# Optimization experiments

Hardware: AMD Instinct MI355X
Metric: run time of the kernel (lower is better)

The kernel has to match this reference:

```python
import jax, jax.numpy as jnp
import numpy as np

H = W = 128
R = 2
H2, W2 = H // R, W // R
TOPK = 3
NSEG = H * W + 1  # segment 0 = background


def _ccl(binary):
    """8-connected component labeling via iterative max-label propagation.
    binary: [H,W] bool. Returns int32 labels, 0 = background; each component
    gets a unique (arbitrary) positive id = max pixel index in the component."""
    idx = jnp.arange(1, H * W + 1, dtype=jnp.int32).reshape(H, W)
    lab0 = jnp.where(binary, idx, 0)

    def cond(c):
        return c[1]

    def body(c):
        lab, _ = c
        nb = jax.lax.reduce_window(lab, jnp.int32(0), jax.lax.max,
                                   (3, 3), (1, 1), 'SAME')  # 3x3 incl. self
        new = jnp.where(binary, nb, 0)
        return new, jnp.any(new != lab)

    lab, _ = jax.lax.while_loop(cond, body, (lab0, jnp.bool_(True)))
    return lab


def _process_one(prob_i, feat_i):
    """prob_i: [1,H,W], feat_i: [Cf,H,W] -> [3*Cf, H2, W2]."""
    p = prob_i[0]
    binary = p > 0.5
    lab = _ccl(binary).reshape(-1)  # [H*W] segment ids

    ones = jnp.ones((H * W,), jnp.float32)
    count = jax.ops.segment_sum(ones, lab, num_segments=NSEG)
    conf_sum = jax.ops.segment_sum(p.reshape(-1), lab, num_segments=NSEG)
    mean_conf = conf_sum / jnp.maximum(count, 1.0)

    rows = jnp.repeat(jnp.arange(H, dtype=jnp.int32), W)
    cols = jnp.tile(jnp.arange(W, dtype=jnp.int32), H)
    min_r = jax.ops.segment_min(rows, lab, num_segments=NSEG)
    max_r = jax.ops.segment_max(rows, lab, num_segments=NSEG)
    min_c = jax.ops.segment_min(cols, lab, num_segments=NSEG)
    max_c = jax.ops.segment_max(cols, lab, num_segments=NSEG)

    valid = (count > 0) & (jnp.arange(NSEG) > 0)
    score = jnp.where(valid, mean_conf, -jnp.inf)
    _, top_idx = jax.lax.top_k(score, TOPK)  # regions sorted by mean confidence
    K = jnp.sum(valid.astype(jnp.int32))     # number of connected regions

    # duplication rules: K==0 -> full image x3; K==1 -> [f0,f0,f0];
    # K==2 -> [f0,f0,f1]; K>=3 -> [f0,f1,f2]
    i0, i1 = top_idx[0], top_idx[1]
    slots = jnp.where(K >= 3, top_idx,
            jnp.where(K == 2, jnp.stack([i0, i0, i1]),
                      jnp.stack([i0, i0, i0])))

    mr = jnp.where(K > 0, min_r[slots], 0)
    Mr = jnp.where(K > 0, max_r[slots] + 1, H)  # bbox half-open, regionprops style
    mc = jnp.where(K > 0, min_c[slots], 0)
    Mc = jnp.where(K > 0, max_c[slots] + 1, W)

    def crop(a, b, c, d):
        # PyTorch nearest interpolate: src = floor(dst * in/out)
        r = a + (jnp.arange(H2) * (b - a)) // H2
        cc = c + (jnp.arange(W2) * (d - c)) // W2
        return feat_i[:, r][:, :, cc]  # [Cf, H2, W2]

    out = jax.vmap(crop)(mr, Mr, mc, Mc)  # [3, Cf, H2, W2]
    return out.reshape(-1, H2, W2)         # [3*Cf, H2, W2]


def setup_inputs() -> dict:
    key = jax.random.key(0)
    k1, k2 = jax.random.split(key)
    prob = jax.random.uniform(k1, (16, 1, H, W), dtype=jnp.float32)
    feat = jax.random.normal(k2, (16, 192, H, W), dtype=jnp.float32)
    return {"prob": prob, "feat": feat}


def reference(prob, feat):
    return jax.vmap(_process_one)(prob, feat)  # [B, 3*Cf, H2, W2]
```

## Files before the change

kernel.cpp:

```cpp
#include <hip/hip_runtime.h>
#include <limits.h>

#define HH 128
#define WW_ 128
#define HW 16384
#define NB 16
#define CF 192
#define H2 64
#define W2 64

#define SH 16
#define NSPI 8
#define NST 128
#define SC 512
#define NCI 4096
#define NLRUN 1024

typedef float vf4 __attribute__((ext_vector_type(4)));
typedef unsigned long long ull;


__device__ inline int uf_find(int* par, int x) {
    volatile int* vp = (volatile int*)par;
    int p = vp[x];
    while (p != x) {
        int g = vp[p];
        vp[x] = g;
        x = g;
        p = vp[x];
    }
    return x;
}

__device__ inline void uf_union(int* par, int a, int b) {
    int ra = uf_find(par, a);
    int rb = uf_find(par, b);
    while (ra != rb) {
        if (ra < rb) { int t = ra; ra = rb; rb = t; }
        int old = atomicCAS(&par[ra], ra, rb);
        if (old == ra) return;
        ra = uf_find(par, old);
        rb = uf_find(par, rb);
    }
}


__device__ inline int getbit2(ull lo, ull hi, int c) {
    return (int)(((c < 64) ? (lo >> c) : (hi >> (c - 64))) & 1ULL);
}

__device__ inline int leading_ones(ull v) {
    ull nv = ~v;
    return (nv == 0ULL) ? 64 : __clzll(nv);
}

__device__ inline int trailing_ones(ull v) {
    ull nv = ~v;
    return (nv == 0ULL) ? 64 : (__ffsll(nv) - 1);
}

__device__ inline int run_start_col(ull lo, ull hi, int c) {
    if (c < 64) {
        int ones = leading_ones(lo << (63 - c));
        return c - ones + 1;
    }
    int ones = leading_ones(hi << (127 - c));
    int rs = c - ones + 1;
    if (rs == 64) rs -= leading_ones(lo);
    return rs;
}

__device__ inline int run_index(ull rs_lo, ull rs_hi, int cs) {
    if (cs < 64)  return __popcll(rs_lo & ((1ULL << cs) - 1ULL));
    if (cs == 64) return __popcll(rs_lo);
    return __popcll(rs_lo) + __popcll(rs_hi & ((1ULL << (cs - 64)) - 1ULL));
}

__device__ inline void top3_ins(float s, int id, int x,
    float& s0, float& s1, float& s2,
    int& i0, int& i1, int& i2,
    int& x0, int& x1, int& x2)
{
    if (x < 0) return;
    if (s > s0 || (s == s0 && id < i0)) {
        s2 = s1; i2 = i1; x2 = x1;
        s1 = s0; i1 = i0; x1 = x0;
        s0 = s;  i0 = id; x0 = x;
    } else if (s > s1 || (s == s1 && id < i1)) {
        s2 = s1; i2 = i1; x2 = x1;
        s1 = s;  i1 = id; x1 = x;
    } else if (s > s2 || (s == s2 && id < i2)) {
        s2 = s;  i2 = id; x2 = x;
    }
}


__global__ __launch_bounds__(256) void stripe_ccl(
    const float* __restrict__ prob,
    int* __restrict__ nlocg, int* __restrict__ gcnt, float* __restrict__ gconf,
    int* __restrict__ gminr, int* __restrict__ gmaxr,
    int* __restrict__ gminc, int* __restrict__ gmaxc,
    int* __restrict__ gmaxid, int* __restrict__ brun, ull* __restrict__ bmask)
{
    __shared__ ull rowm[SH][2];
    __shared__ unsigned char m8[256];
    __shared__ int parent[NLRUN];
    __shared__ int   lcnt[SC];
    __shared__ float lconf[SC];
    __shared__ int lminr[SC], lmaxr[SC], lminc[SC], lmaxc[SC], lmaxid[SC];
    __shared__ int snloc;

    const int g = blockIdx.x;
    const int b = g >> 3, s = g & 7;
    const int row0 = s * SH;
    const int tid = threadIdx.x;
    const int row = tid >> 4;
    const int w0 = (tid & 15) * 8;

    if (tid == 0) snloc = 0;

    const float* p = prob + (size_t)b * HW + (size_t)((row0 + row) << 7) + w0;
    vf4 va = *(const vf4*)p;
    vf4 vb = *(const vf4*)(p + 4);
    int mask8 = 0;
    mask8 |= (va.x > 0.5f) << 0; mask8 |= (va.y > 0.5f) << 1;
    mask8 |= (va.z > 0.5f) << 2; mask8 |= (va.w > 0.5f) << 3;
    mask8 |= (vb.x > 0.5f) << 4; mask8 |= (vb.y > 0.5f) << 5;
    mask8 |= (vb.z > 0.5f) << 6; mask8 |= (vb.w > 0.5f) << 7;
    m8[tid] = (unsigned char)mask8;
    for (int j = tid; j < SC; j += 256) {
        lcnt[j] = 0; lconf[j] = 0.f;
        lminr[j] = INT_MAX; lmaxr[j] = -1;
        lminc[j] = INT_MAX; lmaxc[j] = -1;
        lmaxid[j] = 0;
    }
    __syncthreads();
    if (tid < 32) {
        int r = tid >> 1, half = tid & 1;
        ull v = 0;
        #pragma unroll
        for (int k2 = 0; k2 < 8; ++k2)
            v |= (ull)m8[(r << 4) + (half << 3) + k2] << (k2 * 8);
        rowm[r][half] = v;
    }
    __syncthreads();

    for (int rid = tid; rid < NLRUN; rid += 256) {
        int r = rid >> 6;
        ull lo = rowm[r][0], hi = rowm[r][1];
        ull rs_lo = lo & ~(lo << 1);
        ull rs_hi = hi & ~((hi << 1) | (lo >> 63));
        int nruns = __popcll(rs_lo) + __popcll(rs_hi);
        if ((rid & 63) < nruns) parent[rid] = rid;
    }
    __syncthreads();

    for (int i = tid; i < (SH - 1) * 128; i += 256) {
        int r = 1 + (i >> 7), c = i & 127;
        ull lo = rowm[r][0], hi = rowm[r][1];
        if (!getbit2(lo, hi, c)) continue;
        ull ulo = rowm[r - 1][0], uhi = rowm[r - 1][1];
        int l  = (c > 0)   ? getbit2(lo, hi, c - 1) : 0;
        int rt = (c < 127) ? getbit2(lo, hi, c + 1) : 0;
        int up = getbit2(ulo, uhi, c);
        int ul = (c > 0)   ? getbit2(ulo, uhi, c - 1) : 0;
        int ur = (c < 127) ? getbit2(ulo, uhi, c + 1) : 0;
        bool u1 = up && !(l && ul);
        bool u2 = !up && ul && !l;
        bool u3 = !up && ur && !rt;
        if (!(u1 | u2 | u3)) continue;
        ull rs_lo = lo & ~(lo << 1),   rs_hi = hi & ~((hi << 1) | (lo >> 63));
        ull urs_lo = ulo & ~(ulo << 1), urs_hi = uhi & ~((uhi << 1) | (ulo >> 63));
        int cs = run_start_col(lo, hi, c);
        int rid = (r << 6) + run_index(rs_lo, rs_hi, cs);
        int ub = (r - 1) << 6;
        if (u1) uf_union(parent, rid, ub + run_index(urs_lo, urs_hi, run_start_col(ulo, uhi, c)));
        if (u2) uf_union(parent, rid, ub + run_index(urs_lo, urs_hi, run_start_col(ulo, uhi, c - 1)));
        if (u3) uf_union(parent, rid, ub + run_index(urs_lo, urs_hi, run_start_col(ulo, uhi, c + 1)));
    }
    __syncthreads();

    for (int rid = tid; rid < NLRUN; rid += 256) {
        int r = rid >> 6;
        ull lo = rowm[r][0], hi = rowm[r][1];
        ull rs_lo = lo & ~(lo << 1);
        ull rs_hi = hi & ~((hi << 1) | (lo >> 63));
        int nruns = __popcll(rs_lo) + __popcll(rs_hi);
        if ((rid & 63) < nruns) parent[rid] = uf_find(parent, rid);
    }
    __syncthreads();
    for (int rid = tid; rid < NLRUN; rid += 256) {
        int r = rid >> 6;
        ull lo = rowm[r][0], hi = rowm[r][1];
        ull rs_lo = lo & ~(lo << 1);
        ull rs_hi = hi & ~((hi << 1) | (lo >> 63));
        int nruns = __popcll(rs_lo) + __popcll(rs_hi);
        if ((rid & 63) < nruns && parent[rid] == rid) {
            int idx = atomicAdd(&snloc, 1);
            parent[rid] = NLRUN + idx;
        }
    }
    __syncthreads();

    {
        ull lo = rowm[row][0], hi = rowm[row][1];
        ull rs_lo = lo & ~(lo << 1);
        ull rs_hi = hi & ~((hi << 1) | (lo >> 63));
        const float vv[8] = {va.x, va.y, va.z, va.w, vb.x, vb.y, vb.z, vb.w};
        const int imr = row0 + row;
        int curIdx = -1, aCnt = 0, aMinc = 0, aMaxc = 0, aMaxid = 0;
        float aConf = 0.f;
        bool prevfg = false;
        #pragma unroll
        for (int j = 0; j < 8; ++j) {
            bool fg = (mask8 >> j) & 1;
            if (fg) {
                int c = w0 + j;
                if (!prevfg) {
                    int cs = run_start_col(lo, hi, c);
                    int rid = (row << 6) + run_index(rs_lo, rs_hi, cs);
                    int v = parent[rid];
                    int idx = (v >= NLRUN) ? v - NLRUN : parent[v] - NLRUN;
                    if (idx != curIdx) {
                        if (curIdx >= 0) {
                            atomicAdd(&lcnt[curIdx], aCnt);
                            atomicAdd(&lconf[curIdx], aConf);
                            atomicMin(&lminr[curIdx], imr);
                            atomicMax(&lmaxr[curIdx], imr);
                            atomicMin(&lminc[curIdx], aMinc);
                            atomicMax(&lmaxc[curIdx], aMaxc);
                            atomicMax(&lmaxid[curIdx], aMaxid);
                        }
                        curIdx = idx; aCnt = 0; aConf = 0.f;
                        aMinc = c; aMaxc = c; aMaxid = 0;
                    }
                }
                aCnt++; aConf += vv[j]; aMaxc = c;
                aMaxid = (imr << 7) + c + 1;
            }
            prevfg = fg;
        }
        if (curIdx >= 0) {
            atomicAdd(&lcnt[curIdx], aCnt);
            atomicAdd(&lconf[curIdx], aConf);
            atomicMin(&lminr[curIdx], imr);
            atomicMax(&lmaxr[curIdx], imr);
            atomicMin(&lminc[curIdx], aMinc);
            atomicMax(&lmaxc[curIdx], aMaxc);
            atomicMax(&lmaxid[curIdx], aMaxid);
        }
    }
    __syncthreads();

    const int nl = snloc;
    for (int j = tid; j < nl; j += 256) {
        int d = (g << 9) + j;
        gcnt[d] = lcnt[j];  gconf[d] = lconf[j];
        gminr[d] = lminr[j]; gmaxr[d] = lmaxr[j];
        gminc[d] = lminc[j]; gmaxc[d] = lmaxc[j];
        gmaxid[d] = lmaxid[j];
    }
    if (tid == 0) nlocg[g] = nl;
    if (tid < 128) {
        int br = tid >> 6;
        int j = tid & 63;
        int r = br ? (SH - 1) : 0;
        ull lo = rowm[r][0], hi = rowm[r][1];
        ull rs_lo = lo & ~(lo << 1);
        ull rs_hi = hi & ~((hi << 1) | (lo >> 63));
        int nruns = __popcll(rs_lo) + __popcll(rs_hi);
        if (j < nruns) {
            int rid = (r << 6) + j;
            int v = parent[rid];
            brun[(g << 7) + (br << 6) + j] = (v >= NLRUN) ? v - NLRUN : parent[v] - NLRUN;
        }
        if (j == 0) {
            bmask[(g << 2) + (br << 1) + 0] = lo;
            bmask[(g << 2) + (br << 1) + 1] = hi;
        }
    }
}


__global__ __launch_bounds__(1024) void merge_kernel(
    const int* __restrict__ nlocg, const int* __restrict__ gcnt,
    const float* __restrict__ gconf,
    const int* __restrict__ gminr, const int* __restrict__ gmaxr,
    const int* __restrict__ gminc, const int* __restrict__ gmaxc,
    const int* __restrict__ gmaxid, const int* __restrict__ brun,
    const ull* __restrict__ bmask, int* __restrict__ bbox)
{
    __shared__ int parent2[NCI];
    __shared__ int   cnt2[NCI];
    __shared__ float conf2[NCI];
    __shared__ int minr2[NCI], maxr2[NCI], minc2[NCI], maxc2[NCI], maxid2[NCI];
    __shared__ int sK;
    __shared__ float wss[48];
    __shared__ int wid_[48], wrx[48];

    const int b = blockIdx.x;
    const int tid = threadIdx.x;
    if (tid == 0) sK = 0;
    for (int i = tid; i < NCI; i += 1024) { parent2[i] = i; cnt2[i] = 0; }
    __syncthreads();

    for (int s = 0; s < NSPI; ++s) {
        int g = (b << 3) + s;
        int n = nlocg[g];
        for (int j = tid; j < n; j += 1024) {
            int d = (s << 9) + j, e = (g << 9) + j;
            cnt2[d] = gcnt[e];  conf2[d] = gconf[e];
            minr2[d] = gminr[e]; maxr2[d] = gmaxr[e];
            minc2[d] = gminc[e]; maxc2[d] = gmaxc[e];
            maxid2[d] = gmaxid[e];
        }
    }
    __syncthreads();

    for (int i = tid; i < 7 * 128; i += 1024) {
        int k = 1 + (i >> 7), c = i & 127;
        int gLo = (b << 3) + k, gUp = gLo - 1;
        ull lo = bmask[(gLo << 2) + 0], hi = bmask[(gLo << 2) + 1];
        if (!getbit2(lo, hi, c)) continue;
        ull ulo = bmask[(gUp << 2) + 2], uhi = bmask[(gUp << 2) + 3];
        int l  = (c > 0)   ? getbit2(lo, hi, c - 1) : 0;
        int rt = (c < 127) ? getbit2(lo, hi, c + 1) : 0;
        int up = getbit2(ulo, uhi, c);
        int ul = (c > 0)   ? getbit2(ulo, uhi, c - 1) : 0;
        int ur = (c < 127) ? getbit2(ulo, uhi, c + 1) : 0;
        bool u1 = up && !(l && ul);
        bool u2 = !up && ul && !l;
        bool u3 = !up && ur && !rt;
        if (!(u1 | u2 | u3)) continue;
        ull rs_lo = lo & ~(lo << 1),   rs_hi = hi & ~((hi << 1) | (lo >> 63));
        ull urs_lo = ulo & ~(ulo << 1), urs_hi = uhi & ~((uhi << 1) | (ulo >> 63));
        int cs = run_start_col(lo, hi, c);
        int myid = (k << 9) + brun[(gLo << 7) + run_index(rs_lo, rs_hi, cs)];
        int ubase = (k - 1) << 9;
        if (u1) uf_union(parent2, myid, ubase + brun[(gUp << 7) + 64 + run_index(urs_lo, urs_hi, run_start_col(ulo, uhi, c))]);
        if (u2) uf_union(parent2, myid, ubase + brun[(gUp << 7) + 64 + run_index(urs_lo, urs_hi, run_start_col(ulo, uhi, c - 1))]);
        if (u3) uf_union(parent2, myid, ubase + brun[(gUp << 7) + 64 + run_index(urs_lo, urs_hi, run_start_col(ulo, uhi, c + 1))]);
    }
    __syncthreads();

    for (int i = tid; i < NCI; i += 1024) {
        if (cnt2[i] > 0) {
            int r = uf_find(parent2, i);
            if (r != i) {
                atomicAdd(&cnt2[r], cnt2[i]);   atomicAdd(&conf2[r], conf2[i]);
                atomicMin(&minr2[r], minr2[i]); atomicMax(&maxr2[r], maxr2[i]);
                atomicMin(&minc2[r], minc2[i]); atomicMax(&maxc2[r], maxc2[i]);
                atomicMax(&maxid2[r], maxid2[i]);
            }
        }
    }
    __syncthreads();

    float s0 = -INFINITY, s1 = -INFINITY, s2 = -INFINITY;
    int i0 = INT_MAX, i1 = INT_MAX, i2 = INT_MAX;
    int x0 = -1, x1 = -1, x2 = -1;
    int kc = 0;
    for (int i = tid; i < NCI; i += 1024) {
        if (parent2[i] == i && cnt2[i] > 0) {
            ++kc;
            float sc = conf2[i] / (float)cnt2[i];
            top3_ins(sc, maxid2[i], i, s0, s1, s2, i0, i1, i2, x0, x1, x2);
        }
    }
    for (int off = 32; off; off >>= 1) kc += __shfl_xor(kc, off);
    if ((tid & 63) == 0) atomicAdd(&sK, kc);
    for (int off = 32; off; off >>= 1) {
        float bs0 = __shfl_xor(s0, off), bs1 = __shfl_xor(s1, off), bs2 = __shfl_xor(s2, off);
        int bi0 = __shfl_xor(i0, off), bi1 = __shfl_xor(i1, off), bi2 = __shfl_xor(i2, off);
        int bx0 = __shfl_xor(x0, off), bx1 = __shfl_xor(x1, off), bx2 = __shfl_xor(x2, off);
        top3_ins(bs0, bi0, bx0, s0, s1, s2, i0, i1, i2, x0, x1, x2);
        top3_ins(bs1, bi1, bx1, s0, s1, s2, i0, i1, i2, x0, x1, x2);
        top3_ins(bs2, bi2, bx2, s0, s1, s2, i0, i1, i2, x0, x1, x2);
    }
    if ((tid & 63) == 0) {
        int w = tid >> 6;
        wss[w * 3 + 0] = s0; wid_[w * 3 + 0] = i0; wrx[w * 3 + 0] = x0;
        wss[w * 3 + 1] = s1; wid_[w * 3 + 1] = i1; wrx[w * 3 + 1] = x1;
        wss[w * 3 + 2] = s2; wid_[w * 3 + 2] = i2; wrx[w * 3 + 2] = x2;
    }
    __syncthreads();

    if (tid == 0) {
        float t0 = -INFINITY, t1 = -INFINITY, t2 = -INFINITY;
        int ti0 = INT_MAX, ti1 = INT_MAX, ti2 = INT_MAX;
        int tx0 = -1, tx1 = -1, tx2 = -1;
        for (int t = 0; t < 48; ++t)
            top3_ins(wss[t], wid_[t], wrx[t], t0, t1, t2, ti0, ti1, ti2, tx0, tx1, tx2);
        int K = sK;
        int roots[3];
        if (K >= 3)      { roots[0] = tx0; roots[1] = tx1; roots[2] = tx2; }
        else if (K == 2) { roots[0] = tx0; roots[1] = tx0; roots[2] = tx1; }
        else             { roots[0] = tx0; roots[1] = tx0; roots[2] = tx0; }
        for (int slot = 0; slot < 3; ++slot) {
            int mr, h, mc, w;
            if (K == 0) { mr = 0; h = HH; mc = 0; w = WW_; }
            else {
                int rt = roots[slot];
                mr = minr2[rt]; h = maxr2[rt] + 1 - mr;
                mc = minc2[rt]; w = maxc2[rt] + 1 - mc;
            }
            int* o = bbox + (b * 3 + slot) * 4;
            o[0] = mr; o[1] = h; o[2] = mc; o[3] = w;
        }
    }
}


__global__ __launch_bounds__(256) void crop_kernel(
    const float* __restrict__ feat, const int* __restrict__ bbox,
    float* __restrict__ out)
{
    const int gid = blockIdx.x * 256 + threadIdx.x;
    const int x4 = gid & 15;
    const int y  = (gid >> 4) & 63;
    const int t  = gid >> 10;
    const int c  = t % CF;
    const int bs = t / CF;
    const int* bb = bbox + bs * 4;
    const int mr = bb[0], h = bb[1], mc = bb[2], w = bb[3];
    const int r = mr + ((y * h) >> 6);
    const int bimg = bs / 3;
    const float* row = feat + (((size_t)bimg * CF + c) * HH + r) * WW_;
    const int x = x4 * 4;
    vf4 v;
    v.x = row[mc + (((x + 0) * w) >> 6)];
    v.y = row[mc + (((x + 1) * w) >> 6)];
    v.z = row[mc + (((x + 2) * w) >> 6)];
    v.w = row[mc + (((x + 3) * w) >> 6)];
    __builtin_nontemporal_store(v, (vf4*)out + gid);
}


extern "C" void kernel_launch(void* const* d_in, const int* in_sizes, int n_in,
                              void* d_out, int out_size, void* d_ws, size_t ws_size,
                              hipStream_t stream) {
    const float* prob = (const float*)d_in[0];
    const float* feat = (const float*)d_in[1];
    float* out = (float*)d_out;

    int* ws = (int*)d_ws;
    int* bbox   = ws;
    int* nlocg  = ws + 192;
    int* gcnt   = ws + 320;
    float* gconf = (float*)(ws + 320 + 1 * 65536);
    int* gminr  = ws + 320 + 2 * 65536;
    int* gmaxr  = ws + 320 + 3 * 65536;
    int* gminc  = ws + 320 + 4 * 65536;
    int* gmaxc  = ws + 320 + 5 * 65536;
    int* gmaxid = ws + 320 + 6 * 65536;
    int* brun   = ws + 320 + 7 * 65536;
    ull* bmask  = (ull*)(ws + 320 + 7 * 65536 + 16384);

    hipLaunchKernelGGL(stripe_ccl, dim3(NST), dim3(256), 0, stream,
                       prob, nlocg, gcnt, gconf, gminr, gmaxr, gminc, gmaxc,
                       gmaxid, brun, bmask);
    hipLaunchKernelGGL(merge_kernel, dim3(NB), dim3(1024), 0, stream,
                       nlocg, gcnt, gconf, gminr, gmaxr, gminc, gmaxc,
                       gmaxid, brun, bmask, bbox);
    const int total4 = NB * 3 * CF * H2 * (W2 / 4);
    hipLaunchKernelGGL(crop_kernel, dim3(total4 / 256), dim3(256), 0, stream,
                       feat, bbox, out);
}
```

Before: 351.7 us.

## Fuse CCL, merge and crop into one cooperative kernel with grid syncs

Replaces the three kernel launches (stripe CCL, per-image merge, crop gather) with a single cooperative kernel of 256 blocks of 1024 threads. Grid-wide syncs separate the phases, and a shared-memory union is reused between the stripe and merge stages. This removes launch gaps between the small serial stages. In exchange, the crop phase now runs as a grid-stride loop over only 256 blocks instead of many independent blocks, and the CCL stage idles most of its threads, which may lower memory-level parallelism for the large gather.

```diff
diff --git a/kernel.cpp b/kernel.cpp
--- a/kernel.cpp
+++ b/kernel.cpp
@@ -1,5 +1,8 @@
 #include <hip/hip_runtime.h>
+#include <hip/hip_cooperative_groups.h>
 #include <limits.h>
+
+namespace cg = cooperative_groups;
 
 #define HH 128
 #define WW_ 128
@@ -15,6 +18,8 @@
 #define SC 512
 #define NCI 4096
 #define NLRUN 1024
+#define NBLK 256
+#define NTHR 1024
 
 typedef float vf4 __attribute__((ext_vector_type(4)));
 typedef unsigned long long ull;
@@ -52,11 +57,6 @@
 __device__ inline int leading_ones(ull v) {
     ull nv = ~v;
     return (nv == 0ULL) ? 64 : __clzll(nv);
-}
-
-__device__ inline int trailing_ones(ull v) {
-    ull nv = ~v;
-    return (nv == 0ULL) ? 64 : (__ffsll(nv) - 1);
 }
 
 __device__ inline int run_start_col(ull lo, ull hi, int c) {
@@ -95,344 +95,359 @@
 }
 
 
-__global__ __launch_bounds__(256) void stripe_ccl(
-    const float* __restrict__ prob,
+struct SmA {
+    ull rowm[SH][2];
+    unsigned char m8[256];
+    int parent[NLRUN];
+    int   lcnt[SC];
+    float lconf[SC];
+    int lminr[SC], lmaxr[SC], lminc[SC], lmaxc[SC], lmaxid[SC];
+    int snloc;
+};
+
+struct SmB {
+    int parent2[NCI];
+    int   cnt2[NCI];
+    float conf2[NCI];
+    int minr2[NCI], maxr2[NCI], minc2[NCI], maxc2[NCI], maxid2[NCI];
+    int sK;
+    float wss[48];
+    int wid_[48], wrx[48];
+};
+
+union Sm { SmA a; SmB b; };
+
+
+__global__ __launch_bounds__(NTHR) void fused_kernel(
+    const float* __restrict__ prob, const float* __restrict__ feat,
+    float* __restrict__ out, int* __restrict__ bbox,
     int* __restrict__ nlocg, int* __restrict__ gcnt, float* __restrict__ gconf,
     int* __restrict__ gminr, int* __restrict__ gmaxr,
     int* __restrict__ gminc, int* __restrict__ gmaxc,
     int* __restrict__ gmaxid, int* __restrict__ brun, ull* __restrict__ bmask)
 {
-    __shared__ ull rowm[SH][2];
-    __shared__ unsigned char m8[256];
-    __shared__ int parent[NLRUN];
-    __shared__ int   lcnt[SC];
-    __shared__ float lconf[SC];
-    __shared__ int lminr[SC], lmaxr[SC], lminc[SC], lmaxc[SC], lmaxid[SC];
-    __shared__ int snloc;
-
-    const int g = blockIdx.x;
-    const int b = g >> 3, s = g & 7;
-    const int row0 = s * SH;
+    __shared__ Sm sm;
+    cg::grid_group grid = cg::this_grid();
+    const int blk = blockIdx.x;
     const int tid = threadIdx.x;
-    const int row = tid >> 4;
-    const int w0 = (tid & 15) * 8;
-
-    if (tid == 0) snloc = 0;
-
-    const float* p = prob + (size_t)b * HW + (size_t)((row0 + row) << 7) + w0;
-    vf4 va = *(const vf4*)p;
-    vf4 vb = *(const vf4*)(p + 4);
-    int mask8 = 0;
-    mask8 |= (va.x > 0.5f) << 0; mask8 |= (va.y > 0.5f) << 1;
-    mask8 |= (va.z > 0.5f) << 2; mask8 |= (va.w > 0.5f) << 3;
-    mask8 |= (vb.x > 0.5f) << 4; mask8 |= (vb.y > 0.5f) << 5;
-    mask8 |= (vb.z > 0.5f) << 6; mask8 |= (vb.w > 0.5f) << 7;
-    m8[tid] = (unsigned char)mask8;
-    for (int j = tid; j < SC; j += 256) {
-        lcnt[j] = 0; lconf[j] = 0.f;
-        lminr[j] = INT_MAX; lmaxr[j] = -1;
-        lminc[j] = INT_MAX; lmaxc[j] = -1;
-        lmaxid[j] = 0;
-    }
-    __syncthreads();
-    if (tid < 32) {
-        int r = tid >> 1, half = tid & 1;
-        ull v = 0;
-        #pragma unroll
-        for (int k2 = 0; k2 < 8; ++k2)
-            v |= (ull)m8[(r << 4) + (half << 3) + k2] << (k2 * 8);
-        rowm[r][half] = v;
-    }
-    __syncthreads();
-
-    for (int rid = tid; rid < NLRUN; rid += 256) {
-        int r = rid >> 6;
-        ull lo = rowm[r][0], hi = rowm[r][1];
-        ull rs_lo = lo & ~(lo << 1);
-        ull rs_hi = hi & ~((hi << 1) | (lo >> 63));
-        int nruns = __popcll(rs_lo) + __popcll(rs_hi);
-        if ((rid & 63) < nruns) parent[rid] = rid;
-    }
-    __syncthreads();
-
-    for (int i = tid; i < (SH - 1) * 128; i += 256) {
-        int r = 1 + (i >> 7), c = i & 127;
-        ull lo = rowm[r][0], hi = rowm[r][1];
-        if (!getbit2(lo, hi, c)) continue;
-        ull ulo = rowm[r - 1][0], uhi = rowm[r - 1][1];
-        int l  = (c > 0)   ? getbit2(lo, hi, c - 1) : 0;
-        int rt = (c < 127) ? getbit2(lo, hi, c + 1) : 0;
-        int up = getbit2(ulo, uhi, c);
-        int ul = (c > 0)   ? getbit2(ulo, uhi, c - 1) : 0;
-        int ur = (c < 127) ? getbit2(ulo, uhi, c + 1) : 0;
-        bool u1 = up && !(l && ul);
-        bool u2 = !up && ul && !l;
-        bool u3 = !up && ur && !rt;
-        if (!(u1 | u2 | u3)) continue;
-        ull rs_lo = lo & ~(lo << 1),   rs_hi = hi & ~((hi << 1) | (lo >> 63));
-        ull urs_lo = ulo & ~(ulo << 1), urs_hi = uhi & ~((uhi << 1) | (ulo >> 63));
-        int cs = run_start_col(lo, hi, c);
-        int rid = (r << 6) + run_index(rs_lo, rs_hi, cs);
-        int ub = (r - 1) << 6;
-        if (u1) uf_union(parent, rid, ub + run_index(urs_lo, urs_hi, run_start_col(ulo, uhi, c)));
-        if (u2) uf_union(parent, rid, ub + run_index(urs_lo, urs_hi, run_start_col(ulo, uhi, c - 1)));
-        if (u3) uf_union(parent, rid, ub + run_index(urs_lo, urs_hi, run_start_col(ulo, uhi, c + 1)));
-    }
-    __syncthreads();
-
-    for (int rid = tid; rid < NLRUN; rid += 256) {
-        int r = rid >> 6;
-        ull lo = rowm[r][0], hi = rowm[r][1];
-        ull rs_lo = lo & ~(lo << 1);
-        ull rs_hi = hi & ~((hi << 1) | (lo >> 63));
-        int nruns = __popcll(rs_lo) + __popcll(rs_hi);
-        if ((rid & 63) < nruns) parent[rid] = uf_find(parent, rid);
-    }
-    __syncthreads();
-    for (int rid = tid; rid < NLRUN; rid += 256) {
-        int r = rid >> 6;
-        ull lo = rowm[r][0], hi = rowm[r][1];
-        ull rs_lo = lo & ~(lo << 1);
-        ull rs_hi = hi & ~((hi << 1) | (lo >> 63));
-        int nruns = __popcll(rs_lo) + __popcll(rs_hi);
-        if ((rid & 63) < nruns && parent[rid] == rid) {
-            int idx = atomicAdd(&snloc, 1);
-            parent[rid] = NLRUN + idx;
-        }
-    }
-    __syncthreads();
-
-    {
-        ull lo = rowm[row][0], hi = rowm[row][1];
-        ull rs_lo = lo & ~(lo << 1);
-        ull rs_hi = hi & ~((hi << 1) | (lo >> 63));
-        const float vv[8] = {va.x, va.y, va.z, va.w, vb.x, vb.y, vb.z, vb.w};
-        const int imr = row0 + row;
-        int curIdx = -1, aCnt = 0, aMinc = 0, aMaxc = 0, aMaxid = 0;
-        float aConf = 0.f;
-        bool prevfg = false;
-        #pragma unroll
-        for (int j = 0; j < 8; ++j) {
-            bool fg = (mask8 >> j) & 1;
-            if (fg) {
-                int c = w0 + j;
-                if (!prevfg) {
-                    int cs = run_start_col(lo, hi, c);
-                    int rid = (row << 6) + run_index(rs_lo, rs_hi, cs);
-                    int v = parent[rid];
-                    int idx = (v >= NLRUN) ? v - NLRUN : parent[v] - NLRUN;
-                    if (idx != curIdx) {
-                        if (curIdx >= 0) {
-                            atomicAdd(&lcnt[curIdx], aCnt);
-                            atomicAdd(&lconf[curIdx], aConf);
-                            atomicMin(&lminr[curIdx], imr);
-                            atomicMax(&lmaxr[curIdx], imr);
-                            atomicMin(&lminc[curIdx], aMinc);
-                            atomicMax(&lmaxc[curIdx], aMaxc);
-                            atomicMax(&lmaxid[curIdx], aMaxid);
+
+    if (blk < NST) {
+        SmA& A = sm.a;
+        const int b = blk >> 3, s = blk & 7;
+        const int row0 = s * SH;
+        if (tid == 0) A.snloc = 0;
+
+        int mask8 = 0;
+        vf4 va = {0, 0, 0, 0}, vb = {0, 0, 0, 0};
+        if (tid < 256) {
+            int row = tid >> 4, w0 = (tid & 15) * 8;
+            const float* p = prob + (size_t)b * HW + (size_t)((row0 + row) << 7) + w0;
+            va = *(const vf4*)p;
+            vb = *(const vf4*)(p + 4);
+            mask8 |= (va.x > 0.5f) << 0; mask8 |= (va.y > 0.5f) << 1;
+            mask8 |= (va.z > 0.5f) << 2; mask8 |= (va.w > 0.5f) << 3;
+            mask8 |= (vb.x > 0.5f) << 4; mask8 |= (vb.y > 0.5f) << 5;
+            mask8 |= (vb.z > 0.5f) << 6; mask8 |= (vb.w > 0.5f) << 7;
+            A.m8[tid] = (unsigned char)mask8;
+        }
+        for (int j = tid; j < SC; j += NTHR) {
+            A.lcnt[j] = 0; A.lconf[j] = 0.f;
+            A.lminr[j] = INT_MAX; A.lmaxr[j] = -1;
+            A.lminc[j] = INT_MAX; A.lmaxc[j] = -1;
+            A.lmaxid[j] = 0;
+        }
+        __syncthreads();
+        if (tid < 32) {
+            int r = tid >> 1, half = tid & 1;
+            ull v = 0;
+            #pragma unroll
+            for (int k2 = 0; k2 < 8; ++k2)
+                v |= (ull)A.m8[(r << 4) + (half << 3) + k2] << (k2 * 8);
+            A.rowm[r][half] = v;
+        }
+        __syncthreads();
+
+        {
+            int rid = tid;
+            int r = rid >> 6;
+            ull lo = A.rowm[r][0], hi = A.rowm[r][1];
+            ull rs_lo = lo & ~(lo << 1);
+            ull rs_hi = hi & ~((hi << 1) | (lo >> 63));
+            int nruns = __popcll(rs_lo) + __popcll(rs_hi);
+            if ((rid & 63) < nruns) A.parent[rid] = rid;
+        }
+        __syncthreads();
+
+        for (int i = tid; i < (SH - 1) * 128; i += NTHR) {
+            int r = 1 + (i >> 7), c = i & 127;
+            ull lo = A.rowm[r][0], hi = A.rowm[r][1];
+            if (!getbit2(lo, hi, c)) continue;
+            ull ulo = A.rowm[r - 1][0], uhi = A.rowm[r - 1][1];
+            int l  = (c > 0)   ? getbit2(lo, hi, c - 1) : 0;
+            int rt = (c < 127) ? getbit2(lo, hi, c + 1) : 0;
+            int up = getbit2(ulo, uhi, c);
+            int ul = (c > 0)   ? getbit2(ulo, uhi, c - 1) : 0;
+            int ur = (c < 127) ? getbit2(ulo, uhi, c + 1) : 0;
+            bool u1 = up && !(l && ul);
+            bool u2 = !up && ul && !l;
+            bool u3 = !up && ur && !rt;
+            if (!(u1 | u2 | u3)) continue;
+            ull rs_lo = lo & ~(lo << 1),   rs_hi = hi & ~((hi << 1) | (lo >> 63));
+            ull urs_lo = ulo & ~(ulo << 1), urs_hi = uhi & ~((uhi << 1) | (ulo >> 63));
+            int cs = run_start_col(lo, hi, c);
+            int rid = (r << 6) + run_index(rs_lo, rs_hi, cs);
+            int ub = (r - 1) << 6;
+            if (u1) uf_union(A.parent, rid, ub + run_index(urs_lo, urs_hi, run_start_col(ulo, uhi, c)));
+            if (u2) uf_union(A.parent, rid, ub + run_index(urs_lo, urs_hi, run_start_col(ulo, uhi, c - 1)));
+            if (u3) uf_union(A.parent, rid, ub + run_index(urs_lo, urs_hi, run_start_col(ulo, uhi, c + 1)));
+        }
+        __syncthreads();
+
+        {
+            int rid = tid;
+            int r = rid >> 6;
+            ull lo = A.rowm[r][0], hi = A.rowm[r][1];
+            ull rs_lo = lo & ~(lo << 1);
+            ull rs_hi = hi & ~((hi << 1) | (lo >> 63));
+            int nruns = __popcll(rs_lo) + __popcll(rs_hi);
+            if ((rid & 63) < nruns) A.parent[rid] = uf_find(A.parent, rid);
+        }
+        __syncthreads();
+        {
+            int rid = tid;
+            int r = rid >> 6;
+            ull lo = A.rowm[r][0], hi = A.rowm[r][1];
+            ull rs_lo = lo & ~(lo << 1);
+            ull rs_hi = hi & ~((hi << 1) | (lo >> 63));
+            int nruns = __popcll(rs_lo) + __popcll(rs_hi);
+            if ((rid & 63) < nruns && A.parent[rid] == rid) {
+                int idx = atomicAdd(&A.snloc, 1);
+                A.parent[rid] = NLRUN + idx;
+            }
+        }
+        __syncthreads();
+
+        if (tid < 256) {
+            int row = tid >> 4, w0 = (tid & 15) * 8;
+            ull lo = A.rowm[row][0], hi = A.rowm[row][1];
+            ull rs_lo = lo & ~(lo << 1);
+            ull rs_hi = hi & ~((hi << 1) | (lo >> 63));
+            const float vv[8] = {va.x, va.y, va.z, va.w, vb.x, vb.y, vb.z, vb.w};
+            const int imr = row0 + row;
+            int curIdx = -1, aCnt = 0, aMinc = 0, aMaxc = 0, aMaxid = 0;
+            float aConf = 0.f;
+            bool prevfg = false;
+            #pragma unroll
+            for (int j = 0; j < 8; ++j) {
+                bool fg = (mask8 >> j) & 1;
+                if (fg) {
+                    int c = w0 + j;
+                    if (!prevfg) {
+                        int cs = run_start_col(lo, hi, c);
+                        int rid = (row << 6) + run_index(rs_lo, rs_hi, cs);
+                        int v = A.parent[rid];
+                        int idx = (v >= NLRUN) ? v - NLRUN : A.parent[v] - NLRUN;
+                        if (idx != curIdx) {
+                            if (curIdx >= 0) {
+                                atomicAdd(&A.lcnt[curIdx], aCnt);
+                                atomicAdd(&A.lconf[curIdx], aConf);
+                                atomicMin(&A.lminr[curIdx], imr);
+                                atomicMax(&A.lmaxr[curIdx], imr);
+                                atomicMin(&A.lminc[curIdx], aMinc);
+                                atomicMax(&A.lmaxc[curIdx], aMaxc);
+                                atomicMax(&A.lmaxid[curIdx], aMaxid);
+                            }
+                            curIdx = idx; aCnt = 0; aConf = 0.f;
+                            aMinc = c; aMaxc = c; aMaxid = 0;
                         }
-                        curIdx = idx; aCnt = 0; aConf = 0.f;
-                        aMinc = c; aMaxc = c; aMaxid = 0;
                     }
+                    aCnt++; aConf += vv[j]; aMaxc = c;
+                    aMaxid = (imr << 7) + c + 1;
                 }
-                aCnt++; aConf += vv[j]; aMaxc = c;
-                aMaxid = (imr << 7) + c + 1;
-            }
-            prevfg = fg;
-        }
-        if (curIdx >= 0) {
-            atomicAdd(&lcnt[curIdx], aCnt);
-            atomicAdd(&lconf[curIdx], aConf);
-            atomicMin(&lminr[curIdx], imr);
-            atomicMax(&lmaxr[curIdx], imr);
-            atomicMin(&lminc[curIdx], aMinc);
-            atomicMax(&lmaxc[curIdx], aMaxc);
-            atomicMax(&lmaxid[curIdx], aMaxid);
-        }
-    }
-    __syncthreads();
-
-    const int nl = snloc;
-    for (int j = tid; j < nl; j += 256) {
-        int d = (g << 9) + j;
-        gcnt[d] = lcnt[j];  gconf[d] = lconf[j];
-        gminr[d] = lminr[j]; gmaxr[d] = lmaxr[j];
-        gminc[d] = lminc[j]; gmaxc[d] = lmaxc[j];
-        gmaxid[d] = lmaxid[j];
-    }
-    if (tid == 0) nlocg[g] = nl;
-    if (tid < 128) {
-        int br = tid >> 6;
-        int j = tid & 63;
-        int r = br ? (SH - 1) : 0;
-        ull lo = rowm[r][0], hi = rowm[r][1];
-        ull rs_lo = lo & ~(lo << 1);
-        ull rs_hi = hi & ~((hi << 1) | (lo >> 63));
-        int nruns = __popcll(rs_lo) + __popcll(rs_hi);
-        if (j < nruns) {
-            int rid = (r << 6) + j;
-            int v = parent[rid];
-            brun[(g << 7) + (br << 6) + j] = (v >= NLRUN) ? v - NLRUN : parent[v] - NLRUN;
-        }
-        if (j == 0) {
-            bmask[(g << 2) + (br << 1) + 0] = lo;
-            bmask[(g << 2) + (br << 1) + 1] = hi;
-        }
-    }
-}
-
-
-__global__ __launch_bounds__(1024) void merge_kernel(
-    const int* __restrict__ nlocg, const int* __restrict__ gcnt,
-    const float* __restrict__ gconf,
-    const int* __restrict__ gminr, const int* __restrict__ gmaxr,
-    const int* __restrict__ gminc, const int* __restrict__ gmaxc,
-    const int* __restrict__ gmaxid, const int* __restrict__ brun,
-    const ull* __restrict__ bmask, int* __restrict__ bbox)
-{
-    __shared__ int parent2[NCI];
-    __shared__ int   cnt2[NCI];
-    __shared__ float conf2[NCI];
-    __shared__ int minr2[NCI], maxr2[NCI], minc2[NCI], maxc2[NCI], maxid2[NCI];
-    __shared__ int sK;
-    __shared__ float wss[48];
-    __shared__ int wid_[48], wrx[48];
-
-    const int b = blockIdx.x;
-    const int tid = threadIdx.x;
-    if (tid == 0) sK = 0;
-    for (int i = tid; i < NCI; i += 1024) { parent2[i] = i; cnt2[i] = 0; }
-    __syncthreads();
-
-    for (int s = 0; s < NSPI; ++s) {
-        int g = (b << 3) + s;
-        int n = nlocg[g];
-        for (int j = tid; j < n; j += 1024) {
-            int d = (s << 9) + j, e = (g << 9) + j;
-            cnt2[d] = gcnt[e];  conf2[d] = gconf[e];
-            minr2[d] = gminr[e]; maxr2[d] = gmaxr[e];
-            minc2[d] = gminc[e]; maxc2[d] = gmaxc[e];
-            maxid2[d] = gmaxid[e];
-        }
-    }
-    __syncthreads();
-
-    for (int i = tid; i < 7 * 128; i += 1024) {
-        int k = 1 + (i >> 7), c = i & 127;
-        int gLo = (b << 3) + k, gUp = gLo - 1;
-        ull lo = bmask[(gLo << 2) + 0], hi = bmask[(gLo << 2) + 1];
-        if (!getbit2(lo, hi, c)) continue;
-        ull ulo = bmask[(gUp << 2) + 2], uhi = bmask[(gUp << 2) + 3];
-        int l  = (c > 0)   ? getbit2(lo, hi, c - 1) : 0;
-        int rt = (c < 127) ? getbit2(lo, hi, c + 1) : 0;
-        int up = getbit2(ulo, uhi, c);
-        int ul = (c > 0)   ? getbit2(ulo, uhi, c - 1) : 0;
-        int ur = (c < 127) ? getbit2(ulo, uhi, c + 1) : 0;
-        bool u1 = up && !(l && ul);
-        bool u2 = !up && ul && !l;
-        bool u3 = !up && ur && !rt;
-        if (!(u1 | u2 | u3)) continue;
-        ull rs_lo = lo & ~(lo << 1),   rs_hi = hi & ~((hi << 1) | (lo >> 63));
-        ull urs_lo = ulo & ~(ulo << 1), urs_hi = uhi & ~((uhi << 1) | (ulo >> 63));
-        int cs = run_start_col(lo, hi, c);
-        int myid = (k << 9) + brun[(gLo << 7) + run_index(rs_lo, rs_hi, cs)];
-        int ubase = (k - 1) << 9;
-        if (u1) uf_union(parent2, myid, ubase + brun[(gUp << 7) + 64 + run_index(urs_lo, urs_hi, run_start_col(ulo, uhi, c))]);
-        if (u2) uf_union(parent2, myid, ubase + brun[(gUp << 7) + 64 + run_index(urs_lo, urs_hi, run_start_col(ulo, uhi, c - 1))]);
-        if (u3) uf_union(parent2, myid, ubase + brun[(gUp << 7) + 64 + run_index(urs_lo, urs_hi, run_start_col(ulo, uhi, c + 1))]);
-    }
-    __syncthreads();
-
-    for (int i = tid; i < NCI; i += 1024) {
-        if (cnt2[i] > 0) {
-            int r = uf_find(parent2, i);
-            if (r != i) {
-                atomicAdd(&cnt2[r], cnt2[i]);   atomicAdd(&conf2[r], conf2[i]);
-                atomicMin(&minr2[r], minr2[i]); atomicMax(&maxr2[r], maxr2[i]);
-                atomicMin(&minc2[r], minc2[i]); atomicMax(&maxc2[r], maxc2[i]);
-                atomicMax(&maxid2[r], maxid2[i]);
-            }
-        }
-    }
-    __syncthreads();
-
-    float s0 = -INFINITY, s1 = -INFINITY, s2 = -INFINITY;
-    int i0 = INT_MAX, i1 = INT_MAX, i2 = INT_MAX;
-    int x0 = -1, x1 = -1, x2 = -1;
-    int kc = 0;
-    for (int i = tid; i < NCI; i += 1024) {
-        if (parent2[i] == i && cnt2[i] > 0) {
-            ++kc;
-            float sc = conf2[i] / (float)cnt2[i];
-            top3_ins(sc, maxid2[i], i, s0, s1, s2, i0, i1, i2, x0, x1, x2);
-        }
-    }
-    for (int off = 32; off; off >>= 1) kc += __shfl_xor(kc, off);
-    if ((tid & 63) == 0) atomicAdd(&sK, kc);
-    for (int off = 32; off; off >>= 1) {
-        float bs0 = __shfl_xor(s0, off), bs1 = __shfl_xor(s1, off), bs2 = __shfl_xor(s2, off);
-        int bi0 = __shfl_xor(i0, off), bi1 = __shfl_xor(i1, off), bi2 = __shfl_xor(i2, off);
-        int bx0 = __shfl_xor(x0, off), bx1 = __shfl_xor(x1, off), bx2 = __shfl_xor(x2, off);
-        top3_ins(bs0, bi0, bx0, s0, s1, s2, i0, i1, i2, x0, x1, x2);
-        top3_ins(bs1, bi1, bx1, s0, s1, s2, i0, i1, i2, x0, x1, x2);
-        top3_ins(bs2, bi2, bx2, s0, s1, s2, i0, i1, i2, x0, x1, x2);
-    }
-    if ((tid & 63) == 0) {
-        int w = tid >> 6;
-        wss[w * 3 + 0] = s0; wid_[w * 3 + 0] = i0; wrx[w * 3 + 0] = x0;
-        wss[w * 3 + 1] = s1; wid_[w * 3 + 1] = i1; wrx[w * 3 + 1] = x1;
-        wss[w * 3 + 2] = s2; wid_[w * 3 + 2] = i2; wrx[w * 3 + 2] = x2;
-    }
-    __syncthreads();
-
-    if (tid == 0) {
-        float t0 = -INFINITY, t1 = -INFINITY, t2 = -INFINITY;
-        int ti0 = INT_MAX, ti1 = INT_MAX, ti2 = INT_MAX;
-        int tx0 = -1, tx1 = -1, tx2 = -1;
-        for (int t = 0; t < 48; ++t)
-            top3_ins(wss[t], wid_[t], wrx[t], t0, t1, t2, ti0, ti1, ti2, tx0, tx1, tx2);
-        int K = sK;
-        int roots[3];
-        if (K >= 3)      { roots[0] = tx0; roots[1] = tx1; roots[2] = tx2; }
-        else if (K == 2) { roots[0] = tx0; roots[1] = tx0; roots[2] = tx1; }
-        else             { roots[0] = tx0; roots[1] = tx0; roots[2] = tx0; }
-        for (int slot = 0; slot < 3; ++slot) {
-            int mr, h, mc, w;
-            if (K == 0) { mr = 0; h = HH; mc = 0; w = WW_; }
-            else {
-                int rt = roots[slot];
-                mr = minr2[rt]; h = maxr2[rt] + 1 - mr;
-                mc = minc2[rt]; w = maxc2[rt] + 1 - mc;
-            }
-            int* o = bbox + (b * 3 + slot) * 4;
-            o[0] = mr; o[1] = h; o[2] = mc; o[3] = w;
-        }
-    }
-}
-
-
-__global__ __launch_bounds__(256) void crop_kernel(
-    const float* __restrict__ feat, const int* __restrict__ bbox,
-    float* __restrict__ out)
-{
-    const int gid = blockIdx.x * 256 + threadIdx.x;
-    const int x4 = gid & 15;
-    const int y  = (gid >> 4) & 63;
-    const int t  = gid >> 10;
-    const int c  = t % CF;
-    const int bs = t / CF;
-    const int* bb = bbox + bs * 4;
-    const int mr = bb[0], h = bb[1], mc = bb[2], w = bb[3];
-    const int r = mr + ((y * h) >> 6);
-    const int bimg = bs / 3;
-    const float* row = feat + (((size_t)bimg * CF + c) * HH + r) * WW_;
-    const int x = x4 * 4;
-    vf4 v;
-    v.x = row[mc + (((x + 0) * w) >> 6)];
-    v.y = row[mc + (((x + 1) * w) >> 6)];
-    v.z = row[mc + (((x + 2) * w) >> 6)];
-    v.w = row[mc + (((x + 3) * w) >> 6)];
-    __builtin_nontemporal_store(v, (vf4*)out + gid);
+                prevfg = fg;
+            }
+            if (curIdx >= 0) {
+                atomicAdd(&A.lcnt[curIdx], aCnt);
+                atomicAdd(&A.lconf[curIdx], aConf);
+                atomicMin(&A.lminr[curIdx], imr);
+                atomicMax(&A.lmaxr[curIdx], imr);
+                atomicMin(&A.lminc[curIdx], aMinc);
+                atomicMax(&A.lmaxc[curIdx], aMaxc);
+                atomicMax(&A.lmaxid[curIdx], aMaxid);
+            }
+        }
+        __syncthreads();
+
+        const int nl = A.snloc;
+        for (int j = tid; j < nl; j += NTHR) {
+            int d = (blk << 9) + j;
+            gcnt[d] = A.lcnt[j];  gconf[d] = A.lconf[j];
+            gminr[d] = A.lminr[j]; gmaxr[d] = A.lmaxr[j];
+            gminc[d] = A.lminc[j]; gmaxc[d] = A.lmaxc[j];
+            gmaxid[d] = A.lmaxid[j];
+        }
+        if (tid == 0) nlocg[blk] = nl;
+        if (tid < 128) {
+            int br = tid >> 6;
+            int j = tid & 63;
+            int r = br ? (SH - 1) : 0;
+            ull lo = A.rowm[r][0], hi = A.rowm[r][1];
+            ull rs_lo = lo & ~(lo << 1);
+            ull rs_hi = hi & ~((hi << 1) | (lo >> 63));
+            int nruns = __popcll(rs_lo) + __popcll(rs_hi);
+            if (j < nruns) {
+                int rid = (r << 6) + j;
+                int v = A.parent[rid];
+                brun[(blk << 7) + (br << 6) + j] = (v >= NLRUN) ? v - NLRUN : A.parent[v] - NLRUN;
+            }
+            if (j == 0) {
+                bmask[(blk << 2) + (br << 1) + 0] = lo;
+                bmask[(blk << 2) + (br << 1) + 1] = hi;
+            }
+        }
+    }
+
+    __threadfence();
+    grid.sync();
+    __threadfence();
+
+    if (blk < NB) {
+        SmB& B = sm.b;
+        const int b = blk;
+        if (tid == 0) B.sK = 0;
+        for (int i = tid; i < NCI; i += NTHR) { B.parent2[i] = i; B.cnt2[i] = 0; }
+        __syncthreads();
+
+        for (int s = 0; s < NSPI; ++s) {
+            int g = (b << 3) + s;
+            int n = nlocg[g];
+            for (int j = tid; j < n; j += NTHR) {
+                int d = (s << 9) + j, e = (g << 9) + j;
+                B.cnt2[d] = gcnt[e];  B.conf2[d] = gconf[e];
+                B.minr2[d] = gminr[e]; B.maxr2[d] = gmaxr[e];
+                B.minc2[d] = gminc[e]; B.maxc2[d] = gmaxc[e];
+                B.maxid2[d] = gmaxid[e];
+            }
+        }
+        __syncthreads();
+
+        for (int i = tid; i < 7 * 128; i += NTHR) {
+            int k = 1 + (i >> 7), c = i & 127;
+            int gLo = (b << 3) + k, gUp = gLo - 1;
+            ull lo = bmask[(gLo << 2) + 0], hi = bmask[(gLo << 2) + 1];
+            if (!getbit2(lo, hi, c)) continue;
+            ull ulo = bmask[(gUp << 2) + 2], uhi = bmask[(gUp << 2) + 3];
+            int l  = (c > 0)   ? getbit2(lo, hi, c - 1) : 0;
+            int rt = (c < 127) ? getbit2(lo, hi, c + 1) : 0;
+            int up = getbit2(ulo, uhi, c);
+            int ul = (c > 0)   ? getbit2(ulo, uhi, c - 1) : 0;
+            int ur = (c < 127) ? getbit2(ulo, uhi, c + 1) : 0;
+            bool u1 = up && !(l && ul);
+            bool u2 = !up && ul && !l;
+            bool u3 = !up && ur && !rt;
+            if (!(u1 | u2 | u3)) continue;
+            ull rs_lo = lo & ~(lo << 1),   rs_hi = hi & ~((hi << 1) | (lo >> 63));
+            ull urs_lo = ulo & ~(ulo << 1), urs_hi = uhi & ~((uhi << 1) | (ulo >> 63));
+            int cs = run_start_col(lo, hi, c);
+            int myid = (k << 9) + brun[(gLo << 7) + run_index(rs_lo, rs_hi, cs)];
+            int ubase = (k - 1) << 9;
+            if (u1) uf_union(B.parent2, myid, ubase + brun[(gUp << 7) + 64 + run_index(urs_lo, urs_hi, run_start_col(ulo, uhi, c))]);
+            if (u2) uf_union(B.parent2, myid, ubase + brun[(gUp << 7) + 64 + run_index(urs_lo, urs_hi, run_start_col(ulo, uhi, c - 1))]);
+            if (u3) uf_union(B.parent2, myid, ubase + brun[(gUp << 7) + 64 + run_index(urs_lo, urs_hi, run_start_col(ulo, uhi, c + 1))]);
+        }
+        __syncthreads();
+
+        for (int i = tid; i < NCI; i += NTHR) {
+            if (B.cnt2[i] > 0) {
+                int r = uf_find(B.parent2, i);
+                if (r != i) {
+                    atomicAdd(&B.cnt2[r], B.cnt2[i]);   atomicAdd(&B.conf2[r], B.conf2[i]);
+                    atomicMin(&B.minr2[r], B.minr2[i]); atomicMax(&B.maxr2[r], B.maxr2[i]);
+                    atomicMin(&B.minc2[r], B.minc2[i]); atomicMax(&B.maxc2[r], B.maxc2[i]);
+                    atomicMax(&B.maxid2[r], B.maxid2[i]);
+                }
+            }
+        }
+        __syncthreads();
+
+        float s0 = -INFINITY, s1 = -INFINITY, s2 = -INFINITY;
+        int i0 = INT_MAX, i1 = INT_MAX, i2 = INT_MAX;
+        int x0 = -1, x1 = -1, x2 = -1;
+        int kc = 0;
+        for (int i = tid; i < NCI; i += NTHR) {
+            if (B.parent2[i] == i && B.cnt2[i] > 0) {
+                ++kc;
+                float sc = B.conf2[i] / (float)B.cnt2[i];
+                top3_ins(sc, B.maxid2[i], i, s0, s1, s2, i0, i1, i2, x0, x1, x2);
+            }
+        }
+        for (int off = 32; off; off >>= 1) kc += __shfl_xor(kc, off);
+        if ((tid & 63) == 0) atomicAdd(&B.sK, kc);
+        for (int off = 32; off; off >>= 1) {
+            float bs0 = __shfl_xor(s0, off), bs1 = __shfl_xor(s1, off), bs2 = __shfl_xor(s2, off);
+            int bi0 = __shfl_xor(i0, off), bi1 = __shfl_xor(i1, off), bi2 = __shfl_xor(i2, off);
+            int bx0 = __shfl_xor(x0, off), bx1 = __shfl_xor(x1, off), bx2 = __shfl_xor(x2, off);
+            top3_ins(bs0, bi0, bx0, s0, s1, s2, i0, i1, i2, x0, x1, x2);
+            top3_ins(bs1, bi1, bx1, s0, s1, s2, i0, i1, i2, x0, x1, x2);
+            top3_ins(bs2, bi2, bx2, s0, s1, s2, i0, i1, i2, x0, x1, x2);
+        }
+        if ((tid & 63) == 0) {
+            int w = tid >> 6;
+            B.wss[w * 3 + 0] = s0; B.wid_[w * 3 + 0] = i0; B.wrx[w * 3 + 0] = x0;
+            B.wss[w * 3 + 1] = s1; B.wid_[w * 3 + 1] = i1; B.wrx[w * 3 + 1] = x1;
+            B.wss[w * 3 + 2] = s2; B.wid_[w * 3 + 2] = i2; B.wrx[w * 3 + 2] = x2;
+        }
+        __syncthreads();
+
+        if (tid == 0) {
+            float t0 = -INFINITY, t1 = -INFINITY, t2 = -INFINITY;
+            int ti0 = INT_MAX, ti1 = INT_MAX, ti2 = INT_MAX;
+            int tx0 = -1, tx1 = -1, tx2 = -1;
+            for (int t = 0; t < 48; ++t)
+                top3_ins(B.wss[t], B.wid_[t], B.wrx[t], t0, t1, t2, ti0, ti1, ti2, tx0, tx1, tx2);
+            int K = B.sK;
+            int roots[3];
+            if (K >= 3)      { roots[0] = tx0; roots[1] = tx1; roots[2] = tx2; }
+            else if (K == 2) { roots[0] = tx0; roots[1] = tx0; roots[2] = tx1; }
+            else             { roots[0] = tx0; roots[1] = tx0; roots[2] = tx0; }
+            for (int slot = 0; slot < 3; ++slot) {
+                int mr, h, mc, w;
+                if (K == 0) { mr = 0; h = HH; mc = 0; w = WW_; }
+                else {
+                    int rt = roots[slot];
+                    mr = B.minr2[rt]; h = B.maxr2[rt] + 1 - mr;
+                    mc = B.minc2[rt]; w = B.maxc2[rt] + 1 - mc;
+                }
+                int* o = bbox + (b * 3 + slot) * 4;
+                o[0] = mr; o[1] = h; o[2] = mc; o[3] = w;
+            }
+        }
+    }
+
+    __threadfence();
+    grid.sync();
+    __threadfence();
+
+    const int total4 = NB * 3 * CF * H2 * (W2 / 4);
+    for (int gid = blk * NTHR + tid; gid < total4; gid += NBLK * NTHR) {
+        const int x4 = gid & 15;
+        const int y  = (gid >> 4) & 63;
+        const int t  = gid >> 10;
+        const int c  = t % CF;
+        const int bs = t / CF;
+        const int* bb = bbox + bs * 4;
+        const int mr = bb[0], h = bb[1], mc = bb[2], w = bb[3];
+        const int r = mr + ((y * h) >> 6);
+        const int bimg = bs / 3;
+        const float* row = feat + (((size_t)bimg * CF + c) * HH + r) * WW_;
+        const int x = x4 * 4;
+        vf4 v;
+        v.x = row[mc + (((x + 0) * w) >> 6)];
+        v.y = row[mc + (((x + 1) * w) >> 6)];
+        v.z = row[mc + (((x + 2) * w) >> 6)];
+        v.w = row[mc + (((x + 3) * w) >> 6)];
+        __builtin_nontemporal_store(v, (vf4*)out + gid);
+    }
 }
 
 
@@ -456,13 +471,12 @@
     int* brun   = ws + 320 + 7 * 65536;
     ull* bmask  = (ull*)(ws + 320 + 7 * 65536 + 16384);
 
-    hipLaunchKernelGGL(stripe_ccl, dim3(NST), dim3(256), 0, stream,
-                       prob, nlocg, gcnt, gconf, gminr, gmaxr, gminc, gmaxc,
-                       gmaxid, brun, bmask);
-    hipLaunchKernelGGL(merge_kernel, dim3(NB), dim3(1024), 0, stream,
-                       nlocg, gcnt, gconf, gminr, gmaxr, gminc, gmaxc,
-                       gmaxid, brun, bmask, bbox);
-    const int total4 = NB * 3 * CF * H2 * (W2 / 4);
-    hipLaunchKernelGGL(crop_kernel, dim3(total4 / 256), dim3(256), 0, stream,
-                       feat, bbox, out);
-}
+    void* args[] = {
+        (void*)&prob, (void*)&feat, (void*)&out, (void*)&bbox,
+        (void*)&nlocg, (void*)&gcnt, (void*)&gconf,
+        (void*)&gminr, (void*)&gmaxr, (void*)&gminc, (void*)&gmaxc,
+        (void*)&gmaxid, (void*)&brun, (void*)&bmask
+    };
+    hipLaunchCooperativeKernel((const void*)fused_kernel,
+                               dim3(NBLK), dim3(NTHR), args, 0, stream);
+}
```

New measurement: 624.4 us. +77.5%, slower.
